# Kernel tuning notes

Measured on AMD Instinct MI355X. Metric: run time of the kernel, lower is better.

The kernel has to match this reference:

```python
import jax, jax.numpy as jnp
import numpy as np

B, C, N, K, E = 8, 64, 4096, 16, 64
EPS = 1e-5


def _bn(h, gamma, beta, axes):
    # BatchNorm in training mode: stats over batch+spatial axes, per channel (dim 1)
    m = jnp.mean(h, axis=axes, keepdims=True)
    v = jnp.var(h, axis=axes, keepdims=True)
    shape = (1, -1) + (1,) * (h.ndim - 2)
    return gamma.reshape(shape) * (h - m) * jax.lax.rsqrt(v + EPS) + beta.reshape(shape)


def setup_inputs() -> dict:
    key = jax.random.key(0)
    ks = jax.random.split(key, 8)
    x = jax.random.normal(ks[0], (B, C, N), dtype=jnp.float32)
    idx = jax.random.randint(ks[1], (B, N, K), 0, N, dtype=jnp.int32)
    s1 = 1.0 / np.sqrt(C)
    s2 = 1.0 / np.sqrt(E)
    return {
        "x": x,
        "idx": idx,
        "W1": jax.random.normal(ks[2], (E, C), jnp.float32) * s1,
        "b1": jnp.zeros((E,), jnp.float32),
        "g1": jnp.ones((E,), jnp.float32),
        "be1": jnp.zeros((E,), jnp.float32),
        "W2": jax.random.normal(ks[3], (E, E), jnp.float32) * s2,
        "b2": jnp.zeros((E,), jnp.float32),
        "g2": jnp.ones((E,), jnp.float32),
        "be2": jnp.zeros((E,), jnp.float32),
        "W3": jax.random.normal(ks[4], (E, E), jnp.float32) * s2,
        "b3": jnp.zeros((E,), jnp.float32),
        "g3": jnp.ones((E,), jnp.float32),
        "be3": jnp.zeros((E,), jnp.float32),
    }


def reference(x, idx, W1, b1, g1, be1, W2, b2, g2, be2, W3, b3, g3, be3):
    # gather kNN neighbor features: x[b, :, idx[b]] -> (B, C, N, K)
    nn_feat = jax.vmap(lambda xb, ib: xb[:, ib])(x, idx)
    # edge features: neighbor - center
    h = nn_feat - x[..., None]                                   # (B, C, N, K)
    # Conv2DBlock: two 1x1 conv + BN + ReLU layers
    h = jnp.einsum('bcnk,oc->bonk', h, W1) + b1[:, None, None]
    h = jax.nn.relu(_bn(h, g1, be1, (0, 2, 3)))
    h = jnp.einsum('bcnk,oc->bonk', h, W2) + b2[:, None, None]
    h = jax.nn.relu(_bn(h, g2, be2, (0, 2, 3)))
    # max over neighbors
    h = jnp.max(h, axis=-1)                                      # (B, E, N)
    # Conv1DBlock: 1x1 conv + BN + ReLU
    h = jnp.einsum('bcn,oc->bon', h, W3) + b3[:, None]
    h = jax.nn.relu(_bn(h, g3, be3, (0, 2)))
    return h
```

## Files before the change

### kernel.cpp

```cpp
#include <hip/hip_runtime.h>

#define EPSBN 1e-5f
#define CNT1 524288.0f
#define CNT3 32768.0f
#define NREP 16

typedef short v8s __attribute__((ext_vector_type(8)));
typedef float v16f __attribute__((ext_vector_type(16)));

__device__ __forceinline__ unsigned short f2bf(float f) {
  union { float f; unsigned u; } v; v.f = f;
  unsigned u = v.u;
  u += 0x7fffu + ((u >> 16) & 1u);
  return (unsigned short)(u >> 16);
}
__device__ __forceinline__ unsigned pack2bf(float a, float b) {
  return (unsigned)f2bf(a) | ((unsigned)f2bf(b) << 16);
}
__device__ __forceinline__ float bflo(unsigned u) {
  union { unsigned u; float f; } v; v.u = u << 16; return v.f;
}
__device__ __forceinline__ float bfhi(unsigned u) {
  union { unsigned u; float f; } v; v.u = u & 0xffff0000u; return v.f;
}

__global__ __launch_bounds__(256) void prep(
    const float* __restrict__ x, const float* __restrict__ W1,
    unsigned short* __restrict__ y) {
  __shared__ unsigned short ldsX[64 * 72];
  int blk = blockIdx.x, t = threadIdx.x;
  int b = blk >> 6, n0 = (blk & 63) << 6;
  int tn = t & 63, cg = t >> 6;
#pragma unroll
  for (int i = 0; i < 16; ++i) {
    int c = cg * 16 + i;
    ldsX[tn * 72 + c] = f2bf(x[(((size_t)(b * 64 + c)) << 12) + n0 + tn]);
  }
  __syncthreads();
  int lane = t & 63, w = t >> 6;
  int l31 = lane & 31, lh = lane >> 5;
  int ot = w & 1, ph = w >> 1;
  int o = ot * 32 + l31;
  v16f acc;
#pragma unroll
  for (int i = 0; i < 16; ++i) acc[i] = 0.f;
#pragma unroll
  for (int ks = 0; ks < 4; ++ks) {
    const float* wrow = W1 + o * 64 + ks * 16 + lh * 8;
    float4 wa = *((const float4*)wrow);
    float4 wb = *((const float4*)(wrow + 4));
    v8s wf; unsigned* wu = (unsigned*)&wf;
    wu[0] = pack2bf(wa.x, wa.y); wu[1] = pack2bf(wa.z, wa.w);
    wu[2] = pack2bf(wb.x, wb.y); wu[3] = pack2bf(wb.z, wb.w);
    v8s af = *((const v8s*)&ldsX[(ph * 32 + l31) * 72 + ks * 16 + lh * 8]);
    acc = __builtin_amdgcn_mfma_f32_32x32x16_bf16(af, wf, acc, 0, 0, 0);
  }
#pragma unroll
  for (int i = 0; i < 16; ++i) {
    int row = (i & 3) + ((i >> 2) << 3) + (lh << 2);
    int pt = (b << 12) + n0 + ph * 32 + row;
    y[pt * 64 + o] = f2bf(acc[i]);
  }
}

__global__ __launch_bounds__(256) void p1_stats(
    const unsigned short* __restrict__ y, const int* __restrict__ idx,
    float* __restrict__ S1) {
  __shared__ float bs[64], bq[64];
  int t = threadIdx.x;
  if (t < 64) { bs[t] = 0.f; bq[t] = 0.f; }
  __syncthreads();
  int blk = blockIdx.x;
  int batch = blk & 7, bi = blk >> 3;
  int w = t >> 6, lane = t & 63;
  int ch = (lane & 7) << 3, eg = lane >> 3;
  int ebase = (batch << 16) + bi * 512 + w * 128;
  float ss[8], sq[8];
#pragma unroll
  for (int k = 0; k < 8; ++k) { ss[k] = 0.f; sq[k] = 0.f; }
  for (int it = 0; it < 16; ++it) {
    int p = ebase + it * 8 + eg;
    int j = idx[p];
    int site = p >> 4;
    uint4 uj = *((const uint4*)(y + (((size_t)((batch << 12) + j)) << 6) + ch));
    uint4 ui = *((const uint4*)(y + (((size_t)site) << 6) + ch));
    const unsigned* aj = (const unsigned*)&uj;
    const unsigned* ai = (const unsigned*)&ui;
#pragma unroll
    for (int d = 0; d < 4; ++d) {
      float d0 = bflo(aj[d]) - bflo(ai[d]);
      float d1 = bfhi(aj[d]) - bfhi(ai[d]);
      ss[2 * d] += d0; sq[2 * d] += d0 * d0;
      ss[2 * d + 1] += d1; sq[2 * d + 1] += d1 * d1;
    }
  }
#pragma unroll
  for (int k = 0; k < 8; ++k) {
    ss[k] += __shfl_xor(ss[k], 8);  sq[k] += __shfl_xor(sq[k], 8);
    ss[k] += __shfl_xor(ss[k], 16); sq[k] += __shfl_xor(sq[k], 16);
    ss[k] += __shfl_xor(ss[k], 32); sq[k] += __shfl_xor(sq[k], 32);
  }
  if (lane < 8) {
#pragma unroll
    for (int k = 0; k < 8; ++k) {
      atomicAdd(&bs[ch + k], ss[k]);
      atomicAdd(&bq[ch + k], sq[k]);
    }
  }
  __syncthreads();
  int rep = (blk >> 3) & (NREP - 1);
  if (t < 64) atomicAdd(&S1[rep * 128 + t], bs[t]);
  else if (t < 128) atomicAdd(&S1[rep * 128 + t], bq[t - 64]);
}

__global__ __launch_bounds__(256) void p2_main(
    const unsigned short* __restrict__ y, const int* __restrict__ idx,
    const float* __restrict__ W2f,
    const float* __restrict__ g1, const float* __restrict__ be1,
    const float* __restrict__ S1,
    unsigned short* __restrict__ mnb, unsigned short* __restrict__ mxb,
    float* __restrict__ S2) {
  __shared__ float bs[64], bq[64];
  __shared__ __align__(16) float lA[64];
  __shared__ __align__(16) float lC[64];
  int t = threadIdx.x;
  if (t < 64) {
    bs[t] = 0.f; bq[t] = 0.f;
    float s = 0.f, q = 0.f;
#pragma unroll
    for (int r = 0; r < NREP; ++r) { s += S1[r * 128 + t]; q += S1[r * 128 + 64 + t]; }
    float mean = s / CNT1;
    float var = q / CNT1 - mean * mean;
    float a = g1[t] * rsqrtf(var + EPSBN);
    lA[t] = a; lC[t] = be1[t] - mean * a;
  }
  __syncthreads();
  int blk = blockIdx.x;
  int batch = blk & 7, bi = blk >> 3;
  int w = t >> 6, lane = t & 63;
  int l31 = lane & 31, lh = lane >> 5;
  v8s w2[2][4];
#pragma unroll
  for (int s = 0; s < 2; ++s)
#pragma unroll
    for (int ks = 0; ks < 4; ++ks) {
      const float* wr = W2f + (s * 32 + l31) * 64 + ks * 16 + lh * 8;
      float4 wa = *((const float4*)wr);
      float4 wb = *((const float4*)(wr + 4));
      unsigned* wu = (unsigned*)&w2[s][ks];
      wu[0] = pack2bf(wa.x, wa.y); wu[1] = pack2bf(wa.z, wa.w);
      wu[2] = pack2bf(wb.x, wb.y); wu[3] = pack2bf(wb.z, wb.w);
    }
  float ss0 = 0.f, sq0 = 0.f, ss1 = 0.f, sq1 = 0.f;
  for (int it = 0; it < 8; ++it) {
    int tile = bi * 32 + w * 8 + it;
    int p = (batch << 16) + (tile << 5) + l31;
    int j = idx[p];
    int site = p >> 4;
    const unsigned short* yj = y + (((size_t)((batch << 12) + j)) << 6) + lh * 8;
    const unsigned short* yi = y + (((size_t)site) << 6) + lh * 8;
    v16f b0, b1;
#pragma unroll
    for (int i = 0; i < 16; ++i) { b0[i] = 0.f; b1[i] = 0.f; }
#pragma unroll
    for (int ks = 0; ks < 4; ++ks) {
      uint4 uj = *((const uint4*)(yj + ks * 16));
      uint4 ui = *((const uint4*)(yi + ks * 16));
      float4 a0 = *((const float4*)&lA[ks * 16 + lh * 8]);
      float4 a1 = *((const float4*)&lA[ks * 16 + lh * 8 + 4]);
      float4 c0 = *((const float4*)&lC[ks * 16 + lh * 8]);
      float4 c1 = *((const float4*)&lC[ks * 16 + lh * 8 + 4]);
      float av[8] = {a0.x, a0.y, a0.z, a0.w, a1.x, a1.y, a1.z, a1.w};
      float cv[8] = {c0.x, c0.y, c0.z, c0.w, c1.x, c1.y, c1.z, c1.w};
      const unsigned* jw = (const unsigned*)&uj;
      const unsigned* iw = (const unsigned*)&ui;
      v8s af; unsigned* au = (unsigned*)&af;
#pragma unroll
      for (int d = 0; d < 4; ++d) {
        float e0 = fmaxf((bflo(jw[d]) - bflo(iw[d])) * av[2 * d] + cv[2 * d], 0.f);
        float e1 = fmaxf((bfhi(jw[d]) - bfhi(iw[d])) * av[2 * d + 1] + cv[2 * d + 1], 0.f);
        au[d] = pack2bf(e0, e1);
      }
      b0 = __builtin_amdgcn_mfma_f32_32x32x16_bf16(af, w2[0][ks], b0, 0, 0, 0);
      b1 = __builtin_amdgcn_mfma_f32_32x32x16_bf16(af, w2[1][ks], b1, 0, 0, 0);
    }
    float mx00 = b0[0], mn00 = b0[0], mx01 = b0[8], mn01 = b0[8];
    float mx10 = b1[0], mn10 = b1[0], mx11 = b1[8], mn11 = b1[8];
#pragma unroll
    for (int i = 0; i < 16; ++i) {
      ss0 += b0[i]; sq0 += b0[i] * b0[i];
      ss1 += b1[i]; sq1 += b1[i] * b1[i];
    }
#pragma unroll
    for (int i = 1; i < 8; ++i) {
      mx00 = fmaxf(mx00, b0[i]);     mn00 = fminf(mn00, b0[i]);
      mx01 = fmaxf(mx01, b0[8 + i]); mn01 = fminf(mn01, b0[8 + i]);
      mx10 = fmaxf(mx10, b1[i]);     mn10 = fminf(mn10, b1[i]);
      mx11 = fmaxf(mx11, b1[8 + i]); mn11 = fminf(mn11, b1[8 + i]);
    }
    mx00 = fmaxf(mx00, __shfl_xor(mx00, 32)); mn00 = fminf(mn00, __shfl_xor(mn00, 32));
    mx01 = fmaxf(mx01, __shfl_xor(mx01, 32)); mn01 = fminf(mn01, __shfl_xor(mn01, 32));
    mx10 = fmaxf(mx10, __shfl_xor(mx10, 32)); mn10 = fminf(mn10, __shfl_xor(mn10, 32));
    mx11 = fmaxf(mx11, __shfl_xor(mx11, 32)); mn11 = fminf(mn11, __shfl_xor(mn11, 32));
    int s2 = (batch << 12) + (tile << 1);
    if (lh == 0) {
      mnb[(size_t)(s2 + 0) * 64 + l31] = f2bf(mn00);
      mnb[(size_t)(s2 + 1) * 64 + l31] = f2bf(mn01);
      mnb[(size_t)(s2 + 0) * 64 + 32 + l31] = f2bf(mn10);
      mnb[(size_t)(s2 + 1) * 64 + 32 + l31] = f2bf(mn11);
    } else {
      mxb[(size_t)(s2 + 0) * 64 + l31] = f2bf(mx00);
      mxb[(size_t)(s2 + 1) * 64 + l31] = f2bf(mx01);
      mxb[(size_t)(s2 + 0) * 64 + 32 + l31] = f2bf(mx10);
      mxb[(size_t)(s2 + 1) * 64 + 32 + l31] = f2bf(mx11);
    }
  }
  ss0 += __shfl_xor(ss0, 32); sq0 += __shfl_xor(sq0, 32);
  ss1 += __shfl_xor(ss1, 32); sq1 += __shfl_xor(sq1, 32);
  if (lh == 0) {
    atomicAdd(&bs[l31], ss0); atomicAdd(&bq[l31], sq0);
    atomicAdd(&bs[32 + l31], ss1); atomicAdd(&bq[32 + l31], sq1);
  }
  __syncthreads();
  int rep = blk & (NREP - 1);
  if (t < 64) atomicAdd(&S2[rep * 128 + t], bs[t]);
  else if (t < 128) atomicAdd(&S2[rep * 128 + t], bq[t - 64]);
}

__global__ __launch_bounds__(256, 2) void p3_gemm3(
    const float* __restrict__ W3f,
    const unsigned short* __restrict__ mnb, const unsigned short* __restrict__ mxb,
    const float* __restrict__ g2, const float* __restrict__ be2,
    const float* __restrict__ S2, float* __restrict__ h3, float* __restrict__ S3) {
  __shared__ uint4 ldsA[64 * 9];
  __shared__ float bs[64], bq[64], lA[64], lC[64];
  int t = threadIdx.x;
  if (t < 64) {
    bs[t] = 0.f; bq[t] = 0.f;
    float s = 0.f, q = 0.f;
#pragma unroll
    for (int r = 0; r < NREP; ++r) { s += S2[r * 128 + t]; q += S2[r * 128 + 64 + t]; }
    float mean = s / CNT1;
    float var = q / CNT1 - mean * mean;
    float a = g2[t] * rsqrtf(var + EPSBN);
    lA[t] = a; lC[t] = be2[t] - mean * a;
  }
  __syncthreads();
  int lane = t & 63, wid = t >> 6;
  int rb = wid & 1, ctile = wid >> 1;
  int l31 = lane & 31, lh = lane >> 5;
  int o = ctile * 32 + l31;
  v8s wf[4];
#pragma unroll
  for (int ks = 0; ks < 4; ++ks) {
    const float* wr = W3f + o * 64 + ks * 16 + lh * 8;
    float4 wa = *((const float4*)wr);
    float4 wb = *((const float4*)(wr + 4));
    unsigned* wu = (unsigned*)&wf[ks];
    wu[0] = pack2bf(wa.x, wa.y); wu[1] = pack2bf(wa.z, wa.w);
    wu[2] = pack2bf(wb.x, wb.y); wu[3] = pack2bf(wb.z, wb.w);
  }
  int r = t >> 2, q = t & 3;
  int arow = rb * 32 + l31;
  int s0 = blockIdx.x << 6;
  {
    int site = s0 + r;
    const uint4* mnp = (const uint4*)(mnb + (size_t)site * 64 + q * 16);
    const uint4* mxp = (const uint4*)(mxb + (size_t)site * 64 + q * 16);
    uint4 m0 = mnp[0], m1 = mnp[1], x0 = mxp[0], x1 = mxp[1];
    uint4 ch2[2];
    unsigned* cu = (unsigned*)ch2;
#pragma unroll
    for (int d = 0; d < 8; ++d) {
      unsigned md = (d < 4) ? ((const unsigned*)&m0)[d] : ((const unsigned*)&m1)[d - 4];
      unsigned xd = (d < 4) ? ((const unsigned*)&x0)[d] : ((const unsigned*)&x1)[d - 4];
      int c = q * 16 + 2 * d;
      float a0 = lA[c], a1 = lA[c + 1];
      float s0v = (a0 > 0.f) ? bflo(xd) : bflo(md);
      float s1v = (a1 > 0.f) ? bfhi(xd) : bfhi(md);
      float v0 = fmaxf(a0 * s0v + lC[c], 0.f);
      float v1 = fmaxf(a1 * s1v + lC[c + 1], 0.f);
      cu[d] = pack2bf(v0, v1);
    }
    ldsA[r * 9 + q * 2 + 0] = ch2[0];
    ldsA[r * 9 + q * 2 + 1] = ch2[1];
  }
  __syncthreads();
  v16f acc;
#pragma unroll
  for (int i = 0; i < 16; ++i) acc[i] = 0.f;
#pragma unroll
  for (int ks = 0; ks < 4; ++ks) {
    v8s a = *((const v8s*)&ldsA[arow * 9 + ks * 2 + lh]);
    acc = __builtin_amdgcn_mfma_f32_32x32x16_bf16(a, wf[ks], acc, 0, 0, 0);
  }
  float ssum = 0.f, ssq = 0.f;
#pragma unroll
  for (int i = 0; i < 16; ++i) {
    float vv = acc[i];
    ssum += vv; ssq += vv * vv;
    int row = (i & 3) + ((i >> 2) << 3) + (lh << 2);
    h3[(((size_t)(s0 + rb * 32 + row)) << 6) + o] = vv;
  }
  ssum += __shfl_xor(ssum, 32);
  ssq += __shfl_xor(ssq, 32);
  if (lh == 0) { atomicAdd(&bs[o], ssum); atomicAdd(&bq[o], ssq); }
  __syncthreads();
  int rep = blockIdx.x & (NREP - 1);
  if (t < 64) atomicAdd(&S3[rep * 128 + t], bs[t]);
  else if (t < 128) atomicAdd(&S3[rep * 128 + t], bq[t - 64]);
}

__global__ void k4_out(const float* __restrict__ h3,
                       const float* __restrict__ g3, const float* __restrict__ be3,
                       float* __restrict__ out, const float* __restrict__ S3) {
  __shared__ float lA[64], lC[64];
  __shared__ float tile[64][65];
  int t = threadIdx.x;
  if (t < 64) {
    float s = 0.f, q = 0.f;
#pragma unroll
    for (int r = 0; r < NREP; ++r) { s += S3[r * 128 + t]; q += S3[r * 128 + 64 + t]; }
    float mean = s / CNT3;
    float var = q / CNT3 - mean * mean;
    float a = g3[t] * rsqrtf(var + EPSBN);
    lA[t] = a; lC[t] = be3[t] - mean * a;
  }
  __syncthreads();
  int blk = blockIdx.x;
  int b = blk >> 6, n0 = (blk & 63) << 6;
  int r = t >> 2, q = t & 3;
  const float4* hp = (const float4*)(h3 + (((size_t)((b << 12) + n0 + r)) << 6)) + q * 4;
#pragma unroll
  for (int ii = 0; ii < 4; ++ii) {
    float4 v = hp[ii];
    int c = q * 16 + ii * 4;
    tile[c + 0][r] = fmaxf(v.x * lA[c + 0] + lC[c + 0], 0.f);
    tile[c + 1][r] = fmaxf(v.y * lA[c + 1] + lC[c + 1], 0.f);
    tile[c + 2][r] = fmaxf(v.z * lA[c + 2] + lC[c + 2], 0.f);
    tile[c + 3][r] = fmaxf(v.w * lA[c + 3] + lC[c + 3], 0.f);
  }
  __syncthreads();
  int oo = t >> 2, seg = t & 3;
  float4* dst = (float4*)(out + (((size_t)(b * 64 + oo)) << 12) + n0 + seg * 16);
#pragma unroll
  for (int ii = 0; ii < 4; ++ii) {
    float4 v;
    v.x = tile[oo][seg * 16 + ii * 4 + 0];
    v.y = tile[oo][seg * 16 + ii * 4 + 1];
    v.z = tile[oo][seg * 16 + ii * 4 + 2];
    v.w = tile[oo][seg * 16 + ii * 4 + 3];
    dst[ii] = v;
  }
}

extern "C" void kernel_launch(void* const* d_in, const int* in_sizes, int n_in,
                              void* d_out, int out_size, void* d_ws, size_t ws_size,
                              hipStream_t stream) {
  const float* x = (const float*)d_in[0];
  const int* idx = (const int*)d_in[1];
  const float* W1 = (const float*)d_in[2];
  const float* g1 = (const float*)d_in[4];
  const float* be1 = (const float*)d_in[5];
  const float* W2 = (const float*)d_in[6];
  const float* g2 = (const float*)d_in[8];
  const float* be2 = (const float*)d_in[9];
  const float* W3 = (const float*)d_in[10];
  const float* g3 = (const float*)d_in[12];
  const float* be3 = (const float*)d_in[13];
  float* out = (float*)d_out;

  char* ws = (char*)d_ws;
  unsigned short* y   = (unsigned short*)ws;
  unsigned short* mnb = (unsigned short*)(ws + (4u << 20));
  unsigned short* mxb = (unsigned short*)(ws + (8u << 20));
  float* h3           = (float*)(ws + (12u << 20));
  float* stats        = (float*)(ws + (20u << 20));
  float* S1 = stats;
  float* S2 = stats + NREP * 128;
  float* S3 = stats + 2 * NREP * 128;

  hipMemsetAsync(stats, 0, 3 * NREP * 128 * sizeof(float), stream);
  prep<<<512, 256, 0, stream>>>(x, W1, y);
  p1_stats<<<1024, 256, 0, stream>>>(y, idx, S1);
  p2_main<<<512, 256, 0, stream>>>(y, idx, W2, g1, be1, S1, mnb, mxb, S2);
  p3_gemm3<<<512, 256, 0, stream>>>(W3, mnb, mxb, g2, be2, S2, h3, S3);
  k4_out<<<512, 256, 0, stream>>>(h3, g3, be3, out, S3);
}
```

Before: 140.9 us.

## Fold stats zeroing into prep, double main-kernel grid, interleave batch block mapping

Removes the separate memset launch by having the first 24 blocks of the prep kernel zero the stats buffer. Doubles the grid of the main gather/GEMM kernel and halves each block's tile loop to spread work over more CUs. Adds unroll-2 pragmas to the gather loops and remaps block indices in prep and gemm3 so consecutive blocks cover different batches. Zeroing inside k0 relies on stream ordering, since k1 reads S1 only after k0 finishes.

```diff
diff --git a/kernel.cpp b/kernel.cpp
--- a/kernel.cpp
+++ b/kernel.cpp
@@ -24,20 +24,20 @@
   union { unsigned u; float f; } v; v.u = u & 0xffff0000u; return v.f;
 }
 
-__global__ __launch_bounds__(256) void prep(
-    const float* __restrict__ x, const float* __restrict__ W1,
-    unsigned short* __restrict__ y) {
+__global__ __launch_bounds__(256) void k0_prep(
+    const float* __restrict__ x, const float* __restrict__ W1f,
+    unsigned short* __restrict__ y, float* __restrict__ stats) {
   __shared__ unsigned short ldsX[64 * 72];
   int blk = blockIdx.x, t = threadIdx.x;
-  int b = blk >> 6, n0 = (blk & 63) << 6;
-  int tn = t & 63, cg = t >> 6;
+  if (blk < 24) stats[blk * 256 + t] = 0.f;
+  int b = blk & 7, n0 = (blk >> 3) << 6;
+  int lane = t & 63, w = t >> 6;
 #pragma unroll
   for (int i = 0; i < 16; ++i) {
-    int c = cg * 16 + i;
-    ldsX[tn * 72 + c] = f2bf(x[(((size_t)(b * 64 + c)) << 12) + n0 + tn]);
-  }
-  __syncthreads();
-  int lane = t & 63, w = t >> 6;
+    int c = w * 16 + i;
+    ldsX[lane * 72 + c] = f2bf(x[(((size_t)(b * 64 + c)) << 12) + n0 + lane]);
+  }
+  __syncthreads();
   int l31 = lane & 31, lh = lane >> 5;
   int ot = w & 1, ph = w >> 1;
   int o = ot * 32 + l31;
@@ -46,7 +46,7 @@
   for (int i = 0; i < 16; ++i) acc[i] = 0.f;
 #pragma unroll
   for (int ks = 0; ks < 4; ++ks) {
-    const float* wrow = W1 + o * 64 + ks * 16 + lh * 8;
+    const float* wrow = W1f + o * 64 + ks * 16 + lh * 8;
     float4 wa = *((const float4*)wrow);
     float4 wb = *((const float4*)(wrow + 4));
     v8s wf; unsigned* wu = (unsigned*)&wf;
@@ -63,7 +63,7 @@
   }
 }
 
-__global__ __launch_bounds__(256) void p1_stats(
+__global__ __launch_bounds__(256) void k1_stats(
     const unsigned short* __restrict__ y, const int* __restrict__ idx,
     float* __restrict__ S1) {
   __shared__ float bs[64], bq[64];
@@ -78,6 +78,7 @@
   float ss[8], sq[8];
 #pragma unroll
   for (int k = 0; k < 8; ++k) { ss[k] = 0.f; sq[k] = 0.f; }
+#pragma unroll 2
   for (int it = 0; it < 16; ++it) {
     int p = ebase + it * 8 + eg;
     int j = idx[p];
@@ -113,7 +114,7 @@
   else if (t < 128) atomicAdd(&S1[rep * 128 + t], bq[t - 64]);
 }
 
-__global__ __launch_bounds__(256) void p2_main(
+__global__ __launch_bounds__(256) void k2_main(
     const unsigned short* __restrict__ y, const int* __restrict__ idx,
     const float* __restrict__ W2f,
     const float* __restrict__ g1, const float* __restrict__ be1,
@@ -152,8 +153,9 @@
       wu[2] = pack2bf(wb.x, wb.y); wu[3] = pack2bf(wb.z, wb.w);
     }
   float ss0 = 0.f, sq0 = 0.f, ss1 = 0.f, sq1 = 0.f;
-  for (int it = 0; it < 8; ++it) {
-    int tile = bi * 32 + w * 8 + it;
+#pragma unroll 2
+  for (int it = 0; it < 4; ++it) {
+    int tile = bi * 16 + w * 4 + it;
     int p = (batch << 16) + (tile << 5) + l31;
     int j = idx[p];
     int site = p >> 4;
@@ -227,7 +229,7 @@
   else if (t < 128) atomicAdd(&S2[rep * 128 + t], bq[t - 64]);
 }
 
-__global__ __launch_bounds__(256, 2) void p3_gemm3(
+__global__ __launch_bounds__(256, 2) void k3_gemm3(
     const float* __restrict__ W3f,
     const unsigned short* __restrict__ mnb, const unsigned short* __restrict__ mxb,
     const float* __restrict__ g2, const float* __restrict__ be2,
@@ -262,7 +264,8 @@
   }
   int r = t >> 2, q = t & 3;
   int arow = rb * 32 + l31;
-  int s0 = blockIdx.x << 6;
+  int blk = blockIdx.x;
+  int s0 = ((blk & 7) << 12) + ((blk >> 3) << 6);
   {
     int site = s0 + r;
     const uint4* mnp = (const uint4*)(mnb + (size_t)site * 64 + q * 16);
@@ -306,7 +309,7 @@
   ssq += __shfl_xor(ssq, 32);
   if (lh == 0) { atomicAdd(&bs[o], ssum); atomicAdd(&bq[o], ssq); }
   __syncthreads();
-  int rep = blockIdx.x & (NREP - 1);
+  int rep = blk & (NREP - 1);
   if (t < 64) atomicAdd(&S3[rep * 128 + t], bs[t]);
   else if (t < 128) atomicAdd(&S3[rep * 128 + t], bq[t - 64]);
 }
@@ -380,10 +383,9 @@
   float* S2 = stats + NREP * 128;
   float* S3 = stats + 2 * NREP * 128;
 
-  hipMemsetAsync(stats, 0, 3 * NREP * 128 * sizeof(float), stream);
-  prep<<<512, 256, 0, stream>>>(x, W1, y);
-  p1_stats<<<1024, 256, 0, stream>>>(y, idx, S1);
-  p2_main<<<512, 256, 0, stream>>>(y, idx, W2, g1, be1, S1, mnb, mxb, S2);
-  p3_gemm3<<<512, 256, 0, stream>>>(W3, mnb, mxb, g2, be2, S2, h3, S3);
+  k0_prep<<<512, 256, 0, stream>>>(x, W1, y, stats);
+  k1_stats<<<1024, 256, 0, stream>>>(y, idx, S1);
+  k2_main<<<1024, 256, 0, stream>>>(y, idx, W2, g1, be1, S1, mnb, mxb, S2);
+  k3_gemm3<<<512, 256, 0, stream>>>(W3, mnb, mxb, g2, be2, S2, h3, S3);
   k4_out<<<512, 256, 0, stream>>>(h3, g3, be3, out, S3);
 }
```

New measurement: 141.5 us. About the same (+0.4%).
